# Kernel optimization log

Hardware: AMD Instinct MI355X
Metric: run time of the kernel (lower is better)

The kernel has to match this reference:

```python
import jax, jax.numpy as jnp
import numpy as np

NUM_LATENTS = 32768
NUM_EMBEDDINGS = 1024
EMBEDDING_SIZE = 64


def setup_inputs() -> dict:
    key = jax.random.key(0)
    kx, ke = jax.random.split(key)
    x = jax.random.normal(kx, (NUM_LATENTS * EMBEDDING_SIZE,), dtype=jnp.float32)
    # uniform init in [-limit, limit], limit = sqrt(3/embedding_size) as in the torch module
    limit = float(np.sqrt(3.0 / EMBEDDING_SIZE))
    embeddings = jax.random.uniform(
        ke, (NUM_EMBEDDINGS, EMBEDDING_SIZE), dtype=jnp.float32,
        minval=-limit, maxval=limit)
    return {"x": x, "embeddings": embeddings}


def reference(x, embeddings):
    K, E = embeddings.shape
    x_ = x.reshape(-1, E)  # [L, E]
    # squared distances ||x - e||^2 expanded: faithful to sum((x-e)**2, -1), fused as one GEMM
    d = (
        jnp.sum(x_ * x_, axis=-1, keepdims=True)
        - 2.0 * jnp.einsum('le,ke->lk', x_, embeddings)
        + jnp.sum(embeddings * embeddings, axis=-1)
    )  # [L, K]
    indices = jnp.argmin(d, axis=-1)          # [L]
    quantized = embeddings[indices].reshape(-1)  # [L*E]
    # straight-through estimator: x + (q - stop_grad(x))
    z_hat = x + quantized - jax.lax.stop_gradient(x)
    # outputs mirror the torch dict: z_continuous, z_quantized, z_hat, z_indices
    return x, quantized, z_hat, indices
```

## Files before the change

### kernel.cpp

```cpp
#include <hip/hip_runtime.h>

#define L_TOTAL   32768
#define E_DIM     64
#define K_TOTAL   1024
#define NT_TOTAL  64
#define OUT_STRIDE 2097152
#define XPAD      68
#define BLK_ROWS  64

#define NT_WORDS  1280

typedef _Float16 half_t;
typedef _Float16 half8  __attribute__((ext_vector_type(8)));
typedef float    floatx4 __attribute__((ext_vector_type(4)));

__device__ float g_ebuf[NT_TOTAL * NT_WORDS];

__global__ __launch_bounds__(128)
void vq_swizzle_kernel(const float* __restrict__ emb) {
    __shared__ float s_p[128];
    __shared__ float s_n[16];
    const int nt   = blockIdx.x;
    const int t    = threadIdx.x;
    const int kt   = t >> 6;
    const int lane = t & 63;
    const int q    = lane >> 4;
    const int ln   = lane & 15;

    const float* src = emb + (size_t)(nt * 16 + ln) * E_DIM + kt * 32 + q * 8;
    float4 v0 = *(const float4*)src;
    float4 v1 = *(const float4*)(src + 4);
    float f[8] = {v0.x, v0.y, v0.z, v0.w, v1.x, v1.y, v1.z, v1.w};

    half8 h, l;
    float s = 0.f;
    #pragma unroll
    for (int j = 0; j < 8; ++j) {
        half_t hh = (half_t)f[j];
        half_t ll = (half_t)(f[j] - (float)hh);
        h[j] = hh;
        l[j] = ll;
        s = fmaf(f[j], f[j], s);
    }
    float* rec = g_ebuf + (size_t)nt * NT_WORDS;
    *(half8*)(rec + kt * 256 + lane * 4)       = h;
    *(half8*)(rec + 512 + kt * 256 + lane * 4) = l;

    s_p[t] = s;
    __syncthreads();
    if (t < 16) {
        float n = 0.f;
        #pragma unroll
        for (int u = 0; u < 8; ++u)
            n += s_p[(u >> 2) * 64 + (u & 3) * 16 + t];
        s_n[t] = n;
    }
    __syncthreads();
    if (t < 64) rec[1024 + t] = s_n[t & 15];
}


#define MFMA16(Af, Bf, C) \
    C = __builtin_amdgcn_mfma_f32_16x16x32_f16(Af, Bf, C, 0, 0, 0)

#define COMPUTE_NT(r0, r1, r2, r3, rn, NTv, Tv)                               \
    {                                                                         \
        const int kg_ = (NTv) * 16 + ln;                                      \
        floatx4 kk_[4];                                                       \
        _Pragma("unroll")                                                     \
        for (int rt_ = 0; rt_ < 4; ++rt_) {                                   \
            floatx4 Ca = {0.f,0.f,0.f,0.f}, Cb = {0.f,0.f,0.f,0.f};           \
            MFMA16(A[rt_][0][0], r0, Ca); MFMA16(A[rt_][1][0], r1, Ca);       \
            MFMA16(A[rt_][0][1], r0, Cb); MFMA16(A[rt_][1][1], r1, Cb);       \
            MFMA16(A[rt_][0][0], r2, Cb); MFMA16(A[rt_][1][0], r3, Cb);       \
            _Pragma("unroll")                                                 \
            for (int r = 0; r < 4; ++r)                                       \
                kk_[rt_][r] = fmaf(-2.0f, Ca[r] + Cb[r], rn);                 \
        }                                                                     \
        if ((Tv) < c) {             \
            _Pragma("unroll")                                                 \
            for (int rt_ = 0; rt_ < 4; ++rt_) {                               \
                _Pragma("unroll")                                             \
                for (int r = 0; r < 4; ++r)                                   \
                    if (kk_[rt_][r] < bH[rt_][r]) {                           \
                        bH[rt_][r] = kk_[rt_][r]; iH[rt_][r] = kg_;           \
                    }                                                         \
            }                                                                 \
        } else {                                \
            _Pragma("unroll")                                                 \
            for (int rt_ = 0; rt_ < 4; ++rt_) {                               \
                _Pragma("unroll")                                             \
                for (int r = 0; r < 4; ++r)                                   \
                    if (kk_[rt_][r] < bL[rt_][r]) {                           \
                        bL[rt_][r] = kk_[rt_][r]; iL[rt_][r] = kg_;           \
                    }                                                         \
            }                                                                 \
        }                                                                     \
    }

__global__ __launch_bounds__(256, 2)
void vq_fused_kernel(const float* __restrict__ x,
                     const float* __restrict__ emb,
                     float* __restrict__ out) {
    __shared__ float s_x[BLK_ROWS * XPAD];
    __shared__ float s_best[4][BLK_ROWS];
    __shared__ int   s_bidx[4][BLK_ROWS];
    __shared__ int   s_fin[BLK_ROWS];

    const int tid   = threadIdx.x;
    const int ks    = tid >> 6;
    const int lane  = tid & 63;
    const int q     = lane >> 4;
    const int ln    = lane & 15;
    const int mbase = blockIdx.x * BLK_ROWS;
    const int rot   = blockIdx.x & 15;
    const int nt0   = ks * 16;
    const int c     = 16 - rot;

    {
        const float4* xg = (const float4*)(x + (size_t)mbase * E_DIM);
        #pragma unroll
        for (int i = 0; i < 4; ++i) {
            const int f   = i * 256 + tid;
            const int row = f >> 4;
            const int col = (f & 15) * 4;
            *(float4*)(&s_x[row * XPAD + col]) = xg[f];
        }
    }
    __syncthreads();

    half8 A[4][2][2];
    #pragma unroll
    for (int rt = 0; rt < 4; ++rt) {
        const float* xr = &s_x[(rt * 16 + ln) * XPAD + q * 8];
        #pragma unroll
        for (int kt = 0; kt < 2; ++kt) {
            float4 v0 = *(const float4*)(xr + kt * 32);
            float4 v1 = *(const float4*)(xr + kt * 32 + 4);
            float f[8] = {v0.x, v0.y, v0.z, v0.w, v1.x, v1.y, v1.z, v1.w};
            #pragma unroll
            for (int j = 0; j < 8; ++j) {
                half_t hh = (half_t)f[j];
                half_t ll = (half_t)(f[j] - (float)hh);
                A[rt][kt][0][j] = hh;
                A[rt][kt][1][j] = ll;
            }
        }
    }

    float bH[4][4], bL[4][4];
    int   iH[4][4], iL[4][4];
    #pragma unroll
    for (int rt = 0; rt < 4; ++rt)
        #pragma unroll
        for (int r = 0; r < 4; ++r) {
            bH[rt][r] = 3.402823466e+38f; iH[rt][r] = 0x7fffffff;
            bL[rt][r] = 3.402823466e+38f; iL[rt][r] = 0x7fffffff;
        }

    half8 a0, a1, a2, a3; float ae;
    half8 b0, b1, b2, b3; float be;
    int nt_a, nt_b;
    {
        nt_a = nt0 + (rot & 15);
        const float* rec = g_ebuf + (size_t)nt_a * NT_WORDS;
        a0 = *(const half8*)(rec + lane * 4);
        a1 = *(const half8*)(rec + 256 + lane * 4);
        a2 = *(const half8*)(rec + 512 + lane * 4);
        a3 = *(const half8*)(rec + 768 + lane * 4);
        ae = rec[1024 + lane];
    }

    #pragma unroll 1
    for (int t = 0; t < 16; t += 2) {
        nt_b = nt0 + ((t + 1 + rot) & 15);
        {
            const float* rec = g_ebuf + (size_t)nt_b * NT_WORDS;
            b0 = *(const half8*)(rec + lane * 4);
            b1 = *(const half8*)(rec + 256 + lane * 4);
            b2 = *(const half8*)(rec + 512 + lane * 4);
            b3 = *(const half8*)(rec + 768 + lane * 4);
            be = rec[1024 + lane];
        }
        COMPUTE_NT(a0, a1, a2, a3, ae, nt_a, t);
        if (t + 2 < 16) {
            nt_a = nt0 + ((t + 2 + rot) & 15);
            const float* rec = g_ebuf + (size_t)nt_a * NT_WORDS;
            a0 = *(const half8*)(rec + lane * 4);
            a1 = *(const half8*)(rec + 256 + lane * 4);
            a2 = *(const half8*)(rec + 512 + lane * 4);
            a3 = *(const half8*)(rec + 768 + lane * 4);
            ae = rec[1024 + lane];
        }
        COMPUTE_NT(b0, b1, b2, b3, be, nt_b, t + 1);
    }

    #pragma unroll
    for (int rt = 0; rt < 4; ++rt)
        #pragma unroll
        for (int r = 0; r < 4; ++r)
            if (bH[rt][r] < bL[rt][r]) { bL[rt][r] = bH[rt][r]; iL[rt][r] = iH[rt][r]; }

    #pragma unroll
    for (int o = 1; o < 16; o <<= 1) {
        #pragma unroll
        for (int rt = 0; rt < 4; ++rt)
            #pragma unroll
            for (int r = 0; r < 4; ++r) {
                float ob = __shfl_xor(bL[rt][r], o, 64);
                int   oi = __shfl_xor(iL[rt][r], o, 64);
                if (ob < bL[rt][r] || (ob == bL[rt][r] && oi < iL[rt][r])) {
                    bL[rt][r] = ob; iL[rt][r] = oi;
                }
            }
    }
    if (ln == 0) {
        #pragma unroll
        for (int rt = 0; rt < 4; ++rt)
            #pragma unroll
            for (int r = 0; r < 4; ++r) {
                s_best[ks][rt * 16 + q * 4 + r] = bL[rt][r];
                s_bidx[ks][rt * 16 + q * 4 + r] = iL[rt][r];
            }
    }
    __syncthreads();

    if (tid < BLK_ROWS) {
        float b = 3.402823466e+38f;
        int   i = 0x7fffffff;
        #pragma unroll
        for (int s = 0; s < 4; ++s) {
            float pb = s_best[s][tid];
            int   pi = s_bidx[s][tid];
            if (pb < b || (pb == b && pi < i)) { b = pb; i = pi; }
        }
        s_fin[tid] = i;
        out[3 * (size_t)OUT_STRIDE + mbase + tid] = (float)i;
    }
    __syncthreads();

    {
        const size_t fb = (size_t)mbase * (E_DIM / 4);
        float4* o0 = (float4*)out + fb;
        float4* o1 = (float4*)(out + OUT_STRIDE) + fb;
        float4* o2 = (float4*)(out + 2 * (size_t)OUT_STRIDE) + fb;
        #pragma unroll
        for (int i = 0; i < 4; ++i) {
            const int f   = i * 256 + tid;
            const int row = f >> 4;
            const int col = (f & 15) * 4;
            const float4 xv = *(const float4*)(&s_x[row * XPAD + col]);
            const int idx = s_fin[row];
            const float4 qv = *(const float4*)(emb + (size_t)idx * E_DIM + col);
            float4 z;
            z.x = __fsub_rn(__fadd_rn(xv.x, qv.x), xv.x);
            z.y = __fsub_rn(__fadd_rn(xv.y, qv.y), xv.y);
            z.z = __fsub_rn(__fadd_rn(xv.z, qv.z), xv.z);
            z.w = __fsub_rn(__fadd_rn(xv.w, qv.w), xv.w);
            o0[f] = xv;
            o1[f] = qv;
            o2[f] = z;
        }
    }
}

extern "C" void kernel_launch(void* const* d_in, const int* in_sizes, int n_in,
                              void* d_out, int out_size, void* d_ws, size_t ws_size,
                              hipStream_t stream) {
    const float* x   = (const float*)d_in[0];
    const float* emb = (const float*)d_in[1];
    float* out  = (float*)d_out;
    (void)d_ws; (void)ws_size;

    hipLaunchKernelGGL(vq_swizzle_kernel, dim3(NT_TOTAL), dim3(128), 0, stream,
                       emb);
    hipLaunchKernelGGL(vq_fused_kernel, dim3(L_TOTAL / BLK_ROWS), dim3(256), 0, stream,
                       x, emb, out);
}
```

Before: 86.54 us.

## Fuse embedding fp16 split into main kernel, drop swizzle pre-pass launch

```diff
diff --git a/kernel.cpp b/kernel.cpp
--- a/kernel.cpp
+++ b/kernel.cpp
@@ -8,74 +8,56 @@
 #define XPAD      68
 #define BLK_ROWS  64
 
-#define NT_WORDS  1280
-
 typedef _Float16 half_t;
 typedef _Float16 half8  __attribute__((ext_vector_type(8)));
 typedef float    floatx4 __attribute__((ext_vector_type(4)));
 
-__device__ float g_ebuf[NT_TOTAL * NT_WORDS];
-
-__global__ __launch_bounds__(128)
-void vq_swizzle_kernel(const float* __restrict__ emb) {
-    __shared__ float s_p[128];
-    __shared__ float s_n[16];
-    const int nt   = blockIdx.x;
-    const int t    = threadIdx.x;
-    const int kt   = t >> 6;
-    const int lane = t & 63;
-    const int q    = lane >> 4;
-    const int ln   = lane & 15;
-
-    const float* src = emb + (size_t)(nt * 16 + ln) * E_DIM + kt * 32 + q * 8;
-    float4 v0 = *(const float4*)src;
-    float4 v1 = *(const float4*)(src + 4);
-    float f[8] = {v0.x, v0.y, v0.z, v0.w, v1.x, v1.y, v1.z, v1.w};
-
-    half8 h, l;
-    float s = 0.f;
-    #pragma unroll
-    for (int j = 0; j < 8; ++j) {
-        half_t hh = (half_t)f[j];
-        half_t ll = (half_t)(f[j] - (float)hh);
-        h[j] = hh;
-        l[j] = ll;
-        s = fmaf(f[j], f[j], s);
-    }
-    float* rec = g_ebuf + (size_t)nt * NT_WORDS;
-    *(half8*)(rec + kt * 256 + lane * 4)       = h;
-    *(half8*)(rec + 512 + kt * 256 + lane * 4) = l;
-
-    s_p[t] = s;
-    __syncthreads();
-    if (t < 16) {
-        float n = 0.f;
-        #pragma unroll
-        for (int u = 0; u < 8; ++u)
-            n += s_p[(u >> 2) * 64 + (u & 3) * 16 + t];
-        s_n[t] = n;
-    }
-    __syncthreads();
-    if (t < 64) rec[1024 + t] = s_n[t & 15];
-}
-
 
 #define MFMA16(Af, Bf, C) \
     C = __builtin_amdgcn_mfma_f32_16x16x32_f16(Af, Bf, C, 0, 0, 0)
 
-#define COMPUTE_NT(r0, r1, r2, r3, rn, NTv, Tv)                               \
+#define LOAD_NT(r0, r1, r2, r3, NTv)                                          \
+    {                                                                         \
+        const float* src_ = emb + ((size_t)(NTv) * 16 + ln) * E_DIM + q * 8;  \
+        r0 = *(const float4*)(src_);                \
+        r1 = *(const float4*)(src_ + 4);            \
+        r2 = *(const float4*)(src_ + 32);           \
+        r3 = *(const float4*)(src_ + 36);           \
+    }
+
+#define COMPUTE_NT(r0, r1, r2, r3, NTv, Tv)                                   \
     {                                                                         \
         const int kg_ = (NTv) * 16 + ln;                                      \
+        float f0_[8] = {r0.x, r0.y, r0.z, r0.w, r1.x, r1.y, r1.z, r1.w};      \
+        float f1_[8] = {r2.x, r2.y, r2.z, r2.w, r3.x, r3.y, r3.z, r3.w};      \
+        half8 h0_, l0_, h1_, l1_;                                             \
+        float sn_ = 0.f;                                                      \
+        _Pragma("unroll")                                                     \
+        for (int j = 0; j < 8; ++j) {                                         \
+            half_t hh = (half_t)f0_[j];                                       \
+            h0_[j] = hh;                                                      \
+            l0_[j] = (half_t)(f0_[j] - (float)hh);                            \
+            sn_ = fmaf(f0_[j], f0_[j], sn_);                                  \
+        }                                                                     \
+        _Pragma("unroll")                                                     \
+        for (int j = 0; j < 8; ++j) {                                         \
+            half_t hh = (half_t)f1_[j];                                       \
+            h1_[j] = hh;                                                      \
+            l1_[j] = (half_t)(f1_[j] - (float)hh);                            \
+            sn_ = fmaf(f1_[j], f1_[j], sn_);                                  \
+        }                                                                     \
+        sn_ += __shfl_xor(sn_, 16, 64);                                       \
+        sn_ += __shfl_xor(sn_, 32, 64);                                       \
         floatx4 kk_[4];                                                       \
         _Pragma("unroll")                                                     \
         for (int rt_ = 0; rt_ < 4; ++rt_) {                                   \
             floatx4 Ca = {0.f,0.f,0.f,0.f}, Cb = {0.f,0.f,0.f,0.f};           \
-            MFMA16(A[rt_][0][0], r0, Ca); MFMA16(A[rt_][1][0], r1, Ca);       \
-            MFMA16(A[rt_][0][1], r0, Cb); MFMA16(A[rt_][1][1], r1, Cb);       \
-            MFMA16(A[rt_][0][0], r2, Cb); MFMA16(A[rt_][1][0], r3, Cb);       \
+            MFMA16(A[rt_][0][0], h0_, Ca); MFMA16(A[rt_][1][0], h1_, Ca);     \
+            MFMA16(A[rt_][0][1], h0_, Cb); MFMA16(A[rt_][1][1], h1_, Cb);     \
+            MFMA16(A[rt_][0][0], l0_, Cb); MFMA16(A[rt_][1][0], l1_, Cb);     \
             _Pragma("unroll")                                                 \
             for (int r = 0; r < 4; ++r)                                       \
-                kk_[rt_][r] = fmaf(-2.0f, Ca[r] + Cb[r], rn);                 \
+                kk_[rt_][r] = fmaf(-2.0f, Ca[r] + Cb[r], sn_);                \
         }                                                                     \
         if ((Tv) < c) {             \
             _Pragma("unroll")                                                 \
@@ -158,41 +140,22 @@
             bL[rt][r] = 3.402823466e+38f; iL[rt][r] = 0x7fffffff;
         }
 
-    half8 a0, a1, a2, a3; float ae;
-    half8 b0, b1, b2, b3; float be;
+    float4 a0, a1, a2, a3;
+    float4 b0, b1, b2, b3;
     int nt_a, nt_b;
-    {
-        nt_a = nt0 + (rot & 15);
-        const float* rec = g_ebuf + (size_t)nt_a * NT_WORDS;
-        a0 = *(const half8*)(rec + lane * 4);
-        a1 = *(const half8*)(rec + 256 + lane * 4);
-        a2 = *(const half8*)(rec + 512 + lane * 4);
-        a3 = *(const half8*)(rec + 768 + lane * 4);
-        ae = rec[1024 + lane];
-    }
+    nt_a = nt0 + (rot & 15);
+    LOAD_NT(a0, a1, a2, a3, nt_a);
 
     #pragma unroll 1
     for (int t = 0; t < 16; t += 2) {
         nt_b = nt0 + ((t + 1 + rot) & 15);
-        {
-            const float* rec = g_ebuf + (size_t)nt_b * NT_WORDS;
-            b0 = *(const half8*)(rec + lane * 4);
-            b1 = *(const half8*)(rec + 256 + lane * 4);
-            b2 = *(const half8*)(rec + 512 + lane * 4);
-            b3 = *(const half8*)(rec + 768 + lane * 4);
-            be = rec[1024 + lane];
-        }
-        COMPUTE_NT(a0, a1, a2, a3, ae, nt_a, t);
+        LOAD_NT(b0, b1, b2, b3, nt_b);
+        COMPUTE_NT(a0, a1, a2, a3, nt_a, t);
         if (t + 2 < 16) {
             nt_a = nt0 + ((t + 2 + rot) & 15);
-            const float* rec = g_ebuf + (size_t)nt_a * NT_WORDS;
-            a0 = *(const half8*)(rec + lane * 4);
-            a1 = *(const half8*)(rec + 256 + lane * 4);
-            a2 = *(const half8*)(rec + 512 + lane * 4);
-            a3 = *(const half8*)(rec + 768 + lane * 4);
-            ae = rec[1024 + lane];
-        }
-        COMPUTE_NT(b0, b1, b2, b3, be, nt_b, t + 1);
+            LOAD_NT(a0, a1, a2, a3, nt_a);
+        }
+        COMPUTE_NT(b0, b1, b2, b3, nt_b, t + 1);
     }
 
     #pragma unroll
@@ -272,8 +235,6 @@
     float* out  = (float*)d_out;
     (void)d_ws; (void)ws_size;
 
-    hipLaunchKernelGGL(vq_swizzle_kernel, dim3(NT_TOTAL), dim3(128), 0, stream,
-                       emb);
     hipLaunchKernelGGL(vq_fused_kernel, dim3(L_TOTAL / BLK_ROWS), dim3(256), 0, stream,
                        x, emb, out);
 }
```

Result: slower. 89.60 us (+3.5%).
